# Kernel optimization log

Hardware: AMD Instinct MI355X
Metric: run time of the kernel (lower is better)

The kernel has to match this reference:

```python
import jax, jax.numpy as jnp
import numpy as np

N1 = 50000; N2 = 50000; F = 256; HID = 64; H = 8; DH = HID // H; L = 2; E = 800000


def setup_inputs() -> dict:
    key = jax.random.key(0)
    ks = jax.random.split(key, 20)
    f32 = jnp.float32
    rn = lambda k, shape, s=0.1: jax.random.normal(k, shape, dtype=f32) * s
    inp = {}
    inp['x1'] = jax.random.normal(ks[0], (N1, F), dtype=f32)
    inp['x2'] = jax.random.normal(ks[1], (N2, F), dtype=f32)
    # row 0 = source node ids, row 1 = destination node ids
    inp['edge12'] = jax.random.randint(ks[2], (2, E), 0, N2)  # n1 -> n2
    inp['edge21'] = jax.random.randint(ks[3], (2, E), 0, N1)  # n2 -> n1
    inp['w_in'] = rn(ks[4], (2, HID, F))
    inp['b_in'] = rn(ks[5], (2, HID))
    inp['kw'] = rn(ks[6], (L, 2, HID, HID)); inp['kb'] = rn(ks[7], (L, 2, HID))
    inp['qw'] = rn(ks[8], (L, 2, HID, HID)); inp['qb'] = rn(ks[9], (L, 2, HID))
    inp['vw'] = rn(ks[10], (L, 2, HID, HID)); inp['vb'] = rn(ks[11], (L, 2, HID))
    inp['aw'] = rn(ks[12], (L, 2, HID, HID)); inp['ab'] = rn(ks[13], (L, 2, HID))
    inp['skip'] = jax.random.normal(ks[14], (L, 2), dtype=f32)
    inp['a_rel'] = rn(ks[15], (L, 2, H, DH, DH), 0.3)
    inp['m_rel'] = rn(ks[16], (L, 2, H, DH, DH), 0.3)
    inp['p_rel'] = jnp.ones((L, 2, H), dtype=f32)
    return inp


def _segment_softmax(logits, seg, n):
    # logits: [E, H], seg: [E] destination ids
    m = jax.ops.segment_max(logits, seg, num_segments=n)
    e = jnp.exp(logits - m[seg])
    s = jax.ops.segment_sum(e, seg, num_segments=n)
    return e / s[seg]


def reference(x1, x2, edge12, edge21, w_in, b_in, kw, kb, qw, qb, vw, vb, aw, ab,
              skip, a_rel, m_rel, p_rel):
    scale = jnp.asarray(1.0 / np.sqrt(DH), x1.dtype)

    def kqv(h, l, t):
        k = (h @ kw[l, t].T + kb[l, t]).reshape(-1, H, DH)
        q = (h @ qw[l, t].T + qb[l, t]).reshape(-1, H, DH)
        v = (h @ vw[l, t].T + vb[l, t]).reshape(-1, H, DH)
        return k, q, v

    def message(k_src, v_src, q_dst, edge, ar, mr, pr, n_dst):
        kr = jnp.einsum('nhd,hde->nhe', k_src, ar)   # per-node relation projection
        vr = jnp.einsum('nhd,hde->nhe', v_src, mr)
        s, d = edge[0], edge[1]
        logit = jnp.einsum('ehd,ehd->eh', q_dst[d], kr[s]) * pr[None, :] * scale
        alpha = _segment_softmax(logit, d, n_dst)     # [E, H]
        out = jax.ops.segment_sum(alpha[:, :, None] * vr[s], d, num_segments=n_dst)
        return out.reshape(n_dst, HID)

    def update(o, h, l, t):
        o = jax.nn.gelu(o, approximate=False) @ aw[l, t].T + ab[l, t]
        beta = jax.nn.sigmoid(skip[l, t])
        return beta * o + (1.0 - beta) * h

    # per-node-type input Linear + ReLU stem
    h1 = jax.nn.relu(x1 @ w_in[0].T + b_in[0])
    h2 = jax.nn.relu(x2 @ w_in[1].T + b_in[1])

    outs1, outs2 = [], []
    for l in range(L):
        k1, q1, v1 = kqv(h1, l, 0)
        k2, q2, v2 = kqv(h2, l, 1)
        o2 = message(k1, v1, q2, edge12, a_rel[l, 0], m_rel[l, 0], p_rel[l, 0], h2.shape[0])
        o1 = message(k2, v2, q1, edge21, a_rel[l, 1], m_rel[l, 1], p_rel[l, 1], h1.shape[0])
        h1 = update(o1, h1, l, 0)
        h2 = update(o2, h2, l, 1)
        outs1.append(h1)
        outs2.append(h2)

    Em = jnp.concatenate(outs1, axis=1)  # [N1, HID*L]
    Ed = jnp.concatenate(outs2, axis=1)  # [N2, HID*L]
    return Em, Ed
```

## Files before the change

### kernel.cpp

```cpp
#include <hip/hip_runtime.h>
#include <hip/hip_bf16.h>
#include <hip/hip_fp8.h>
#include <math.h>

typedef __attribute__((ext_vector_type(8))) short bf16x8;
typedef __attribute__((ext_vector_type(4))) float f32x4;
typedef __attribute__((ext_vector_type(2))) float f32x2;
typedef __attribute__((ext_vector_type(4))) unsigned int u32x4;
typedef __attribute__((ext_vector_type(4))) int i32x4;
typedef unsigned short ushort_t;
typedef unsigned char uchar_t;

#define BUCKET_SHIFT 6
#define BUCKET_CAP   64

__device__ inline short f2b(float f) {
    __hip_bfloat16 h = __float2bfloat16(f);
    return __builtin_bit_cast(short, h);
}
__device__ inline float b2f(unsigned short u) {
    return __builtin_bit_cast(float, (unsigned int)u << 16);
}
__device__ inline float blo(unsigned int w) {
    return __builtin_bit_cast(float, w << 16);
}
__device__ inline float bhi(unsigned int w) {
    return __builtin_bit_cast(float, w & 0xffff0000u);
}
__device__ inline uchar_t f2f8(float f) {
    __hip_fp8_e4m3 h(f);
    return (uchar_t)h.__x;
}
__device__ inline float gelu1(float o) {
    return 0.5f * o * (1.f + erff(o * 0.70710678118654752f));
}

__global__ __launch_bounds__(256) void prep_kernel(
    const float* __restrict__ w_in,
    const float* __restrict__ kw, const float* __restrict__ kb,
    const float* __restrict__ qw, const float* __restrict__ qb,
    const float* __restrict__ vw, const float* __restrict__ vb,
    const float* __restrict__ aw,
    const float* __restrict__ a_rel, const float* __restrict__ m_rel,
    const float* __restrict__ p_rel,
    short* __restrict__ wstem, short* __restrict__ Wcat,
    float* __restrict__ Bcat, short* __restrict__ Awb)
{
    int bid = blockIdx.x, tid = threadIdx.x;
    if (bid >= 4) {
        int t = bid - 4;
        for (int i = tid; i < 16384; i += 256)
            wstem[t * 16384 + i] = f2b(w_in[t * 16384 + i]);
        return;
    }
    int base = bid;
    const float* KW = kw + base * 4096;
    const float* QW = qw + base * 4096;
    const float* VW = vw + base * 4096;
    const float* AR = a_rel + base * 512;
    const float* MR = m_rel + base * 512;
    const float* PR = p_rel + base * 8;
    short* WC = Wcat + base * 12288;
    float* BC = Bcat + base * 192;

    for (int i = tid; i < 4096; i += 256) WC[i] = f2b(QW[i]);
    for (int i = tid; i < 4096; i += 256) {
        int out = i >> 6, in = i & 63;
        int h = out >> 3, e = out & 7;
        float s = PR[h] * 0.35355339059327373f;
        float acc = 0.f;
        #pragma unroll
        for (int d = 0; d < 8; ++d) acc += KW[(h * 8 + d) * 64 + in] * AR[h * 64 + d * 8 + e];
        WC[4096 + i] = f2b(acc * s);
    }
    for (int i = tid; i < 4096; i += 256) {
        int out = i >> 6, in = i & 63;
        int h = out >> 3, e = out & 7;
        float acc = 0.f;
        #pragma unroll
        for (int d = 0; d < 8; ++d) acc += VW[(h * 8 + d) * 64 + in] * MR[h * 64 + d * 8 + e];
        WC[8192 + i] = f2b(acc);
    }
    if (tid < 64) {
        BC[tid] = qb[base * 64 + tid];
    } else if (tid < 128) {
        int out = tid - 64;
        int h = out >> 3, e = out & 7;
        float s = PR[h] * 0.35355339059327373f;
        float acc = 0.f;
        #pragma unroll
        for (int d = 0; d < 8; ++d) acc += kb[base * 64 + h * 8 + d] * AR[h * 64 + d * 8 + e];
        BC[64 + out] = acc * s;
    } else if (tid < 192) {
        int out = tid - 128;
        int h = out >> 3, e = out & 7;
        float acc = 0.f;
        #pragma unroll
        for (int d = 0; d < 8; ++d) acc += vb[base * 64 + h * 8 + d] * MR[h * 64 + d * 8 + e];
        BC[128 + out] = acc;
    }
    for (int i = tid; i < 4096; i += 256) Awb[base * 4096 + i] = f2b(aw[base * 4096 + i]);
}

__global__ __launch_bounds__(256) void stem2_mfma(
    const float* __restrict__ X1, const float* __restrict__ X2,
    const short* __restrict__ Wb, const float* __restrict__ B1, const float* __restrict__ B2,
    short* __restrict__ H1, short* __restrict__ H2, int N1, int N2, int nt1)
{
    const float* X; const short* Wsrc; const float* B; short* Hb; int N; int tb;
    if (blockIdx.x < nt1) { X = X1; Wsrc = Wb;         B = B1; Hb = H1; N = N1; tb = blockIdx.x; }
    else                  { X = X2; Wsrc = Wb + 16384; B = B2; Hb = H2; N = N2; tb = blockIdx.x - nt1; }
    __shared__ short Ws[64 * 256];
    int tid = threadIdx.x;
    #pragma unroll
    for (int k = 0; k < 8; ++k) {
        int u = tid + k * 256;
        int row = u >> 5, c = u & 31;
        u32x4 v = *reinterpret_cast<const u32x4*>(Wsrc + row * 256 + c * 8);
        *reinterpret_cast<u32x4*>(&Ws[row * 256 + ((c ^ (row & 7)) << 3)]) = v;
    }
    __syncthreads();
    int w = tid >> 6, l = tid & 63;
    int g = l >> 4, q = l & 15;
    int row = tb * 64 + w * 16 + q;
    bool rok = row < N;
    f32x4 acc[4] = {};
    const float* xr = X + (size_t)row * 256 + g * 8;
    #pragma unroll
    for (int s = 0; s < 8; ++s) {
        bf16x8 a = {};
        if (rok) {
            float4 x0 = *reinterpret_cast<const float4*>(xr + s * 32);
            float4 x1 = *reinterpret_cast<const float4*>(xr + s * 32 + 4);
            a[0] = f2b(x0.x); a[1] = f2b(x0.y); a[2] = f2b(x0.z); a[3] = f2b(x0.w);
            a[4] = f2b(x1.x); a[5] = f2b(x1.y); a[6] = f2b(x1.z); a[7] = f2b(x1.w);
        }
        #pragma unroll
        for (int n = 0; n < 4; ++n) {
            int br = n * 16 + q;
            int c = s * 4 + g;
            bf16x8 b = *reinterpret_cast<bf16x8*>(&Ws[br * 256 + ((c ^ (br & 7)) << 3)]);
            acc[n] = __builtin_amdgcn_mfma_f32_16x16x32_bf16(a, b, acc[n], 0, 0, 0);
        }
    }
    int orow0 = tb * 64 + w * 16 + g * 4;
    #pragma unroll
    for (int n = 0; n < 4; ++n) {
        int col = n * 16 + q;
        float bias = B[col];
        #pragma unroll
        for (int r = 0; r < 4; ++r) {
            int orow = orow0 + r;
            if (orow < N)
                Hb[(size_t)orow * 64 + col] = f2b(fmaxf(acc[n][r] + bias, 0.f));
        }
    }
}

__global__ __launch_bounds__(256) void kqv2_mfma(
    const short* __restrict__ H1, const short* __restrict__ Wc1, const float* __restrict__ Bc1,
    short* __restrict__ Q1, uchar_t* __restrict__ KV1, int N1,
    const short* __restrict__ H2, const short* __restrict__ Wc2, const float* __restrict__ Bc2,
    short* __restrict__ Q2, uchar_t* __restrict__ KV2, int N2, int nt1)
{
    const short* Hb; const short* Wcat; const float* Bcat; short* Qb; uchar_t* KV; int N; int tb;
    if (blockIdx.x < nt1) { Hb = H1; Wcat = Wc1; Bcat = Bc1; Qb = Q1; KV = KV1; N = N1; tb = blockIdx.x; }
    else                  { Hb = H2; Wcat = Wc2; Bcat = Bc2; Qb = Q2; KV = KV2; N = N2; tb = blockIdx.x - nt1; }
    __shared__ short Ws[192 * 64];
    int tid = threadIdx.x;
    #pragma unroll
    for (int k = 0; k < 6; ++k) {
        int u = tid + k * 256;
        int row = u >> 3, c = u & 7;
        u32x4 v = *reinterpret_cast<const u32x4*>(Wcat + row * 64 + c * 8);
        *reinterpret_cast<u32x4*>(&Ws[row * 64 + ((c ^ (row & 7)) << 3)]) = v;
    }
    __syncthreads();
    int w = tid >> 6, l = tid & 63;
    int g = l >> 4, q = l & 15;
    int arow = tb * 64 + w * 16 + q;
    bool rok = arow < N;
    bf16x8 a0 = {}, a1 = {};
    if (rok) {
        a0 = *reinterpret_cast<const bf16x8*>(Hb + (size_t)arow * 64 + g * 8);
        a1 = *reinterpret_cast<const bf16x8*>(Hb + (size_t)arow * 64 + 32 + g * 8);
    }
    f32x4 acc[12] = {};
    #pragma unroll
    for (int n = 0; n < 12; ++n) {
        int br = n * 16 + q;
        bf16x8 b0 = *reinterpret_cast<bf16x8*>(&Ws[br * 64 + ((0 * 4 + g) ^ (br & 7)) * 8]);
        acc[n] = __builtin_amdgcn_mfma_f32_16x16x32_bf16(a0, b0, acc[n], 0, 0, 0);
        bf16x8 b1 = *reinterpret_cast<bf16x8*>(&Ws[br * 64 + ((1 * 4 + g) ^ (br & 7)) * 8]);
        acc[n] = __builtin_amdgcn_mfma_f32_16x16x32_bf16(a1, b1, acc[n], 0, 0, 0);
    }
    int orow0 = tb * 64 + w * 16 + g * 4;
    #pragma unroll
    for (int n = 0; n < 12; ++n) {
        int col = n * 16 + q;
        float bias = Bcat[col];
        #pragma unroll
        for (int r = 0; r < 4; ++r) {
            int orow = orow0 + r;
            if (orow < N) {
                float v = acc[n][r] + bias;
                if (n < 4)      Qb[(size_t)orow * 64 + col]              = f2b(v);
                else if (n < 8) KV[(size_t)orow * 128 + 2 * (col - 64)]  = f2f8(v);
                else            KV[(size_t)orow * 128 + 2 * (col - 128) + 1] = f2f8(v);
            }
        }
    }
}

__global__ __launch_bounds__(256) void bucket8d_kernel(
    const int* __restrict__ e12, const int* __restrict__ e21,
    int* __restrict__ cnt12, int* __restrict__ cnt21,
    ushort_t* __restrict__ cs12, ushort_t* __restrict__ cs21,
    int E, int N1, int N2, int G)
{
    int grp = blockIdx.x & 7;
    int blk = blockIdx.x >> 3;
    bool dirA = grp < 4;
    const int* srcp = dirA ? e12 : e21;
    const int* dstp = dirA ? (e12 + E) : (e21 + E);
    int* cnt = dirA ? cnt12 : cnt21;
    ushort_t* cs = dirA ? cs12 : cs21;
    int Nn = dirA ? N2 : N1;
    int qr = grp & 3;
    int range = (Nn + 3) >> 2;
    int lo = qr * range, hi = lo + range;
    int E4 = E >> 2;
    int stride = G * 256;
    for (int v = blk * 256 + threadIdx.x; v < E4; v += stride) {
        i32x4 d4 = __builtin_nontemporal_load(reinterpret_cast<const i32x4*>(dstp) + v);
        int base = v * 4;
        if (d4.x >= lo && d4.x < hi) { int p = atomicAdd(&cnt[d4.x], 1); if (p < BUCKET_CAP) cs[((size_t)d4.x << BUCKET_SHIFT) + p] = (ushort_t)srcp[base]; }
        if (d4.y >= lo && d4.y < hi) { int p = atomicAdd(&cnt[d4.y], 1); if (p < BUCKET_CAP) cs[((size_t)d4.y << BUCKET_SHIFT) + p] = (ushort_t)srcp[base + 1]; }
        if (d4.z >= lo && d4.z < hi) { int p = atomicAdd(&cnt[d4.z], 1); if (p < BUCKET_CAP) cs[((size_t)d4.z << BUCKET_SHIFT) + p] = (ushort_t)srcp[base + 2]; }
        if (d4.w >= lo && d4.w < hi) { int p = atomicAdd(&cnt[d4.w], 1); if (p < BUCKET_CAP) cs[((size_t)d4.w << BUCKET_SHIFT) + p] = (ushort_t)srcp[base + 3]; }
    }
    int tail = E & 3;
    if (blk == 0 && threadIdx.x < tail) {
        int i = E - tail + threadIdx.x;
        int d = dstp[i];
        if (d >= lo && d < hi) { int p = atomicAdd(&cnt[d], 1); if (p < BUCKET_CAP) cs[((size_t)d << BUCKET_SHIFT) + p] = (ushort_t)srcp[i]; }
    }
}

__global__ __launch_bounds__(256) void gather64_kernel(
    const int* __restrict__ cntA, const ushort_t* __restrict__ csA,
    const short* __restrict__ QA, const uchar_t* __restrict__ KVA, short* __restrict__ GA, int NA,
    const int* __restrict__ cntB, const ushort_t* __restrict__ csB,
    const short* __restrict__ QB, const uchar_t* __restrict__ KVB, short* __restrict__ GB, int NB)
{
    int grp = blockIdx.x & 7;
    int localBlock = (blockIdx.x >> 3) * 4 + (grp & 3);
    const int* cnt; const ushort_t* cs; const short* Qb; const uchar_t* KV; short* G; int N;
    if (grp < 4) { cnt = cntA; cs = csA; Qb = QA; KV = KVA; G = GA; N = NA; }
    else         { cnt = cntB; cs = csB; Qb = QB; KV = KVB; G = GB; N = NB; }
    int d = localBlock * 4 + (threadIdx.x >> 6);
    if (d >= N) return;
    int lane = threadIdx.x & 63;
    int j = lane & 7;
    int sub = lane >> 3;
    int deg = min(cnt[d], BUCKET_CAP);
    u32x4 qw = *reinterpret_cast<const u32x4*>(Qb + (size_t)d * 64 + 8 * j);
    float q0 = blo(qw.x), q1 = bhi(qw.x), q2 = blo(qw.y), q3 = bhi(qw.y);
    float q4 = blo(qw.z), q5 = bhi(qw.z), q6 = blo(qw.w), q7 = bhi(qw.w);
    float a0 = 0.f, a1 = 0.f, a2 = 0.f, a3 = 0.f;
    float a4 = 0.f, a5 = 0.f, a6 = 0.f, a7 = 0.f, den = 0.f;
    int idv = (lane < deg) ? (int)cs[((size_t)d << BUCKET_SHIFT) + lane] : 0;
    for (int i = 0; i < deg; i += 8) {
        int idx = i + sub;
        bool valid = idx < deg;
        int s = __shfl(idv, valid ? idx : 0);
        u32x4 wv = *reinterpret_cast<const u32x4*>(KV + (size_t)s * 128 + 16 * j);
        f32x2 p0 = __builtin_amdgcn_cvt_pk_f32_fp8((int)wv.x, false);
        f32x2 p1 = __builtin_amdgcn_cvt_pk_f32_fp8((int)wv.x, true);
        f32x2 p2 = __builtin_amdgcn_cvt_pk_f32_fp8((int)wv.y, false);
        f32x2 p3 = __builtin_amdgcn_cvt_pk_f32_fp8((int)wv.y, true);
        f32x2 p4 = __builtin_amdgcn_cvt_pk_f32_fp8((int)wv.z, false);
        f32x2 p5 = __builtin_amdgcn_cvt_pk_f32_fp8((int)wv.z, true);
        f32x2 p6 = __builtin_amdgcn_cvt_pk_f32_fp8((int)wv.w, false);
        f32x2 p7 = __builtin_amdgcn_cvt_pk_f32_fp8((int)wv.w, true);
        float t = q0 * p0[0];
        t = fmaf(q1, p1[0], t);
        t = fmaf(q2, p2[0], t);
        t = fmaf(q3, p3[0], t);
        t = fmaf(q4, p4[0], t);
        t = fmaf(q5, p5[0], t);
        t = fmaf(q6, p6[0], t);
        t = fmaf(q7, p7[0], t);
        float e = valid ? __expf(t) : 0.f;
        den += e;
        a0 = fmaf(e, p0[1], a0);
        a1 = fmaf(e, p1[1], a1);
        a2 = fmaf(e, p2[1], a2);
        a3 = fmaf(e, p3[1], a3);
        a4 = fmaf(e, p4[1], a4);
        a5 = fmaf(e, p5[1], a5);
        a6 = fmaf(e, p6[1], a6);
        a7 = fmaf(e, p7[1], a7);
    }
    #pragma unroll
    for (int m = 8; m <= 32; m <<= 1) {
        a0 += __shfl_xor(a0, m); a1 += __shfl_xor(a1, m);
        a2 += __shfl_xor(a2, m); a3 += __shfl_xor(a3, m);
        a4 += __shfl_xor(a4, m); a5 += __shfl_xor(a5, m);
        a6 += __shfl_xor(a6, m); a7 += __shfl_xor(a7, m);
        den += __shfl_xor(den, m);
    }
    if (lane < 8) {
        float r = (den > 0.f) ? 1.f / den : 0.f;
        float g0 = gelu1(a0 * r), g1 = gelu1(a1 * r), g2 = gelu1(a2 * r), g3 = gelu1(a3 * r);
        float g4 = gelu1(a4 * r), g5 = gelu1(a5 * r), g6 = gelu1(a6 * r), g7 = gelu1(a7 * r);
        u32x4 pw;
        pw.x = ((unsigned int)(unsigned short)f2b(g0)) | (((unsigned int)(unsigned short)f2b(g1)) << 16);
        pw.y = ((unsigned int)(unsigned short)f2b(g2)) | (((unsigned int)(unsigned short)f2b(g3)) << 16);
        pw.z = ((unsigned int)(unsigned short)f2b(g4)) | (((unsigned int)(unsigned short)f2b(g5)) << 16);
        pw.w = ((unsigned int)(unsigned short)f2b(g6)) | (((unsigned int)(unsigned short)f2b(g7)) << 16);
        *reinterpret_cast<u32x4*>(G + (size_t)d * 64 + 8 * j) = pw;
    }
}

__global__ __launch_bounds__(256) void updkqv_mfma(
    const short* __restrict__ G1, const short* __restrict__ Aw1, const float* __restrict__ Ab1,
    const float* __restrict__ sk1, short* __restrict__ H1, float* __restrict__ Out1, int N1,
    const short* __restrict__ G2, const short* __restrict__ Aw2, const float* __restrict__ Ab2,
    const float* __restrict__ sk2, short* __restrict__ H2, float* __restrict__ Out2, int N2,
    const short* __restrict__ Wc1n, const float* __restrict__ Bc1n,
    short* __restrict__ Q1, uchar_t* __restrict__ KV1,
    const short* __restrict__ Wc2n, const float* __restrict__ Bc2n,
    short* __restrict__ Q2, uchar_t* __restrict__ KV2,
    int nt1, int outColOff)
{
    const short* G; const short* Awb; const float* Ab; const float* skipp;
    short* Hb; float* Out; int N; int tb;
    const short* Wcat; const float* Bcat; short* Qb; uchar_t* KV;
    if (blockIdx.x < nt1) {
        G = G1; Awb = Aw1; Ab = Ab1; skipp = sk1; Hb = H1; Out = Out1; N = N1; tb = blockIdx.x;
        Wcat = Wc1n; Bcat = Bc1n; Qb = Q1; KV = KV1;
    } else {
        G = G2; Awb = Aw2; Ab = Ab2; skipp = sk2; Hb = H2; Out = Out2; N = N2; tb = blockIdx.x - nt1;
        Wcat = Wc2n; Bcat = Bc2n; Qb = Q2; KV = KV2;
    }
    __shared__ short Ws[192 * 64];
    __shared__ short hs[64][64];
    int tid = threadIdx.x;
    #pragma unroll
    for (int k = 0; k < 6; ++k) {
        int u = tid + k * 256;
        int row = u >> 3, c = u & 7;
        u32x4 v = *reinterpret_cast<const u32x4*>(Wcat + row * 64 + c * 8);
        *reinterpret_cast<u32x4*>(&Ws[row * 64 + ((c ^ (row & 7)) << 3)]) = v;
    }
    int w = tid >> 6, l = tid & 63;
    int g = l >> 4, q = l & 15;
    bf16x8 bfw[4][2];
    #pragma unroll
    for (int n = 0; n < 4; ++n)
        #pragma unroll
        for (int s = 0; s < 2; ++s)
            bfw[n][s] = *reinterpret_cast<const bf16x8*>(Awb + (n * 16 + q) * 64 + s * 32 + g * 8);
    float beta = 1.f / (1.f + __expf(-skipp[0]));
    int arow = tb * 64 + w * 16 + q;
    bool rok = arow < N;
    bf16x8 ua0 = {}, ua1 = {};
    if (rok) {
        ua0 = *reinterpret_cast<const bf16x8*>(G + (size_t)arow * 64 + g * 8);
        ua1 = *reinterpret_cast<const bf16x8*>(G + (size_t)arow * 64 + 32 + g * 8);
    }
    f32x4 uacc[4] = {};
    #pragma unroll
    for (int n = 0; n < 4; ++n) {
        uacc[n] = __builtin_amdgcn_mfma_f32_16x16x32_bf16(ua0, bfw[n][0], uacc[n], 0, 0, 0);
        uacc[n] = __builtin_amdgcn_mfma_f32_16x16x32_bf16(ua1, bfw[n][1], uacc[n], 0, 0, 0);
    }
    int orow0 = tb * 64 + w * 16 + g * 4;
    int lrow0 = w * 16 + g * 4;
    #pragma unroll
    for (int n = 0; n < 4; ++n) {
        int col = n * 16 + q;
        float bias = Ab[col];
        #pragma unroll
        for (int r = 0; r < 4; ++r) {
            int orow = orow0 + r;
            if (orow < N) {
                float hold = b2f(((const unsigned short*)Hb)[(size_t)orow * 64 + col]);
                float hnew = beta * (uacc[n][r] + bias) + (1.f - beta) * hold;
                short hb16 = f2b(hnew);
                Out[(size_t)orow * 128 + outColOff + col] = hnew;
                Hb[(size_t)orow * 64 + col] = hb16;
                hs[lrow0 + r][col] = hb16;
            } else {
                hs[lrow0 + r][col] = 0;
            }
        }
    }
    __syncthreads();
    bf16x8 a0 = *reinterpret_cast<const bf16x8*>(&hs[w * 16 + q][g * 8]);
    bf16x8 a1 = *reinterpret_cast<const bf16x8*>(&hs[w * 16 + q][32 + g * 8]);
    f32x4 acc[12] = {};
    #pragma unroll
    for (int n = 0; n < 12; ++n) {
        int br = n * 16 + q;
        bf16x8 b0 = *reinterpret_cast<bf16x8*>(&Ws[br * 64 + ((0 * 4 + g) ^ (br & 7)) * 8]);
        acc[n] = __builtin_amdgcn_mfma_f32_16x16x32_bf16(a0, b0, acc[n], 0, 0, 0);
        bf16x8 b1 = *reinterpret_cast<bf16x8*>(&Ws[br * 64 + ((1 * 4 + g) ^ (br & 7)) * 8]);
        acc[n] = __builtin_amdgcn_mfma_f32_16x16x32_bf16(a1, b1, acc[n], 0, 0, 0);
    }
    #pragma unroll
    for (int n = 0; n < 12; ++n) {
        int col = n * 16 + q;
        float bias = Bcat[col];
        #pragma unroll
        for (int r = 0; r < 4; ++r) {
            int orow = orow0 + r;
            if (orow < N) {
                float v = acc[n][r] + bias;
                if (n < 4)      Qb[(size_t)orow * 64 + col]              = f2b(v);
                else if (n < 8) KV[(size_t)orow * 128 + 2 * (col - 64)]  = f2f8(v);
                else            KV[(size_t)orow * 128 + 2 * (col - 128) + 1] = f2f8(v);
            }
        }
    }
}

__global__ __launch_bounds__(256) void update2_mfma(
    const short* __restrict__ G1, const short* __restrict__ Aw1, const float* __restrict__ Ab1,
    const float* __restrict__ sk1, short* __restrict__ H1, float* __restrict__ Out1, int N1,
    const short* __restrict__ G2, const short* __restrict__ Aw2, const float* __restrict__ Ab2,
    const float* __restrict__ sk2, short* __restrict__ H2, float* __restrict__ Out2, int N2,
    int nt1, int outColOff)
{
    const short* G; const short* Awb; const float* Ab; const float* skipp;
    short* Hb; float* Out; int N; int tb;
    if (blockIdx.x < nt1) { G = G1; Awb = Aw1; Ab = Ab1; skipp = sk1; Hb = H1; Out = Out1; N = N1; tb = blockIdx.x; }
    else                  { G = G2; Awb = Aw2; Ab = Ab2; skipp = sk2; Hb = H2; Out = Out2; N = N2; tb = blockIdx.x - nt1; }
    int tid = threadIdx.x;
    int w = tid >> 6, l = tid & 63;
    int g = l >> 4, q = l & 15;
    bf16x8 bf[4][2];
    #pragma unroll
    for (int n = 0; n < 4; ++n)
        #pragma unroll
        for (int s = 0; s < 2; ++s)
            bf[n][s] = *reinterpret_cast<const bf16x8*>(Awb + (n * 16 + q) * 64 + s * 32 + g * 8);
    float beta = 1.f / (1.f + __expf(-skipp[0]));
    int arow = tb * 64 + w * 16 + q;
    bool rok = arow < N;
    bf16x8 a0 = {}, a1 = {};
    if (rok) {
        a0 = *reinterpret_cast<const bf16x8*>(G + (size_t)arow * 64 + g * 8);
        a1 = *reinterpret_cast<const bf16x8*>(G + (size_t)arow * 64 + 32 + g * 8);
    }
    f32x4 acc[4] = {};
    #pragma unroll
    for (int n = 0; n < 4; ++n) {
        acc[n] = __builtin_amdgcn_mfma_f32_16x16x32_bf16(a0, bf[n][0], acc[n], 0, 0, 0);
        acc[n] = __builtin_amdgcn_mfma_f32_16x16x32_bf16(a1, bf[n][1], acc[n], 0, 0, 0);
    }
    int orow0 = tb * 64 + w * 16 + g * 4;
    #pragma unroll
    for (int n = 0; n < 4; ++n) {
        int col = n * 16 + q;
        float bias = Ab[col];
        #pragma unroll
        for (int r = 0; r < 4; ++r) {
            int orow = orow0 + r;
            if (orow < N) {
                float hold = b2f(((const unsigned short*)Hb)[(size_t)orow * 64 + col]);
                float hnew = beta * (acc[n][r] + bias) + (1.f - beta) * hold;
                Out[(size_t)orow * 128 + outColOff + col] = hnew;
                Hb[(size_t)orow * 64 + col] = f2b(hnew);
            }
        }
    }
}

extern "C" void kernel_launch(void* const* d_in, const int* in_sizes, int n_in,
                              void* d_out, int out_size, void* d_ws, size_t ws_size,
                              hipStream_t stream) {
    const float* x1    = (const float*)d_in[0];
    const float* x2    = (const float*)d_in[1];
    const int*   e12   = (const int*)d_in[2];
    const int*   e21   = (const int*)d_in[3];
    const float* w_in  = (const float*)d_in[4];
    const float* b_in  = (const float*)d_in[5];
    const float* kw    = (const float*)d_in[6];
    const float* kb    = (const float*)d_in[7];
    const float* qw    = (const float*)d_in[8];
    const float* qb    = (const float*)d_in[9];
    const float* vw    = (const float*)d_in[10];
    const float* vb    = (const float*)d_in[11];
    const float* aw    = (const float*)d_in[12];
    const float* ab    = (const float*)d_in[13];
    const float* skip  = (const float*)d_in[14];
    const float* a_rel = (const float*)d_in[15];
    const float* m_rel = (const float*)d_in[16];
    const float* p_rel = (const float*)d_in[17];

    int N1 = in_sizes[0] / 256;
    int N2 = in_sizes[1] / 256;
    int E  = in_sizes[2] / 2;

    float* out = (float*)d_out;

    char* wsp = (char*)d_ws;
    auto alloc = [&](size_t bytes) { void* p = wsp; wsp += (bytes + 255) & ~(size_t)255; return p; };
    short* hb1   = (short*)alloc((size_t)N1 * 64 * 2);
    short* hb2   = (short*)alloc((size_t)N2 * 64 * 2);
    short* qb1   = (short*)alloc((size_t)N1 * 64 * 2);
    short* qb2   = (short*)alloc((size_t)N2 * 64 * 2);
    uchar_t* kv1 = (uchar_t*)alloc((size_t)N1 * 128);
    uchar_t* kv2 = (uchar_t*)alloc((size_t)N2 * 128);
    short* g1    = (short*)alloc((size_t)N1 * 64 * 2);
    short* g2    = (short*)alloc((size_t)N2 * 64 * 2);
    short* wstem = (short*)alloc(2 * 16384 * 2);
    short* WcatB = (short*)alloc(4 * 12288 * 2);
    float* BcatB = (float*)alloc(4 * 192 * 4);
    short* AwbB  = (short*)alloc(4 * 4096 * 2);
    int* cnts    = (int*)alloc((size_t)(N1 + N2) * 4);
    int* cnt12   = cnts;
    int* cnt21   = cnts + N2;
    ushort_t* csr12 = (ushort_t*)alloc(((size_t)N2 << BUCKET_SHIFT) * 2);
    ushort_t* csr21 = (ushort_t*)alloc(((size_t)N1 << BUCKET_SHIFT) * 2);

    const int BLK = 256;
    int nt1 = (N1 + 63) / 64;
    int nt2 = (N2 + 63) / 64;
    const int G8 = 512;

    prep_kernel<<<6, BLK, 0, stream>>>(w_in, kw, kb, qw, qb, vw, vb, aw,
                                       a_rel, m_rel, p_rel, wstem, WcatB, BcatB, AwbB);

    hipMemsetAsync(cnts, 0, (size_t)(N1 + N2) * 4, stream);
    bucket8d_kernel<<<8 * G8, BLK, 0, stream>>>(e12, e21, cnt12, cnt21,
                                                csr12, csr21, E, N1, N2, G8);

    stem2_mfma<<<nt1 + nt2, BLK, 0, stream>>>(x1, x2, wstem, b_in, b_in + 64,
                                              hb1, hb2, N1, N2, nt1);

    int bA = (N2 + 3) / 4;
    int bB = (N1 + 3) / 4;
    int bmax = bA > bB ? bA : bB;
    int nlb = (bmax + 3) / 4;
    int gblocks = 8 * nlb;

    kqv2_mfma<<<nt1 + nt2, BLK, 0, stream>>>(
        hb1, WcatB + (size_t)0 * 12288, BcatB + (size_t)0 * 192, qb1, kv1, N1,
        hb2, WcatB + (size_t)1 * 12288, BcatB + (size_t)1 * 192, qb2, kv2, N2, nt1);

    gather64_kernel<<<gblocks, BLK, 0, stream>>>(
        cnt12, csr12, qb2, kv1, g2, N2,
        cnt21, csr21, qb1, kv2, g1, N1);

    updkqv_mfma<<<nt1 + nt2, BLK, 0, stream>>>(
        g1, AwbB + (size_t)0 * 4096, ab + (size_t)0 * 64, skip + 0, hb1, out, N1,
        g2, AwbB + (size_t)1 * 4096, ab + (size_t)1 * 64, skip + 1, hb2,
        out + (size_t)N1 * 128, N2,
        WcatB + (size_t)2 * 12288, BcatB + (size_t)2 * 192, qb1, kv1,
        WcatB + (size_t)3 * 12288, BcatB + (size_t)3 * 192, qb2, kv2,
        nt1, 0);

    gather64_kernel<<<gblocks, BLK, 0, stream>>>(
        cnt12, csr12, qb2, kv1, g2, N2,
        cnt21, csr21, qb1, kv2, g1, N1);

    update2_mfma<<<nt1 + nt2, BLK, 0, stream>>>(
        g1, AwbB + (size_t)2 * 4096, ab + (size_t)2 * 64, skip + 2, hb1, out, N1,
        g2, AwbB + (size_t)3 * 4096, ab + (size_t)3 * 64, skip + 3, hb2,
        out + (size_t)N1 * 128, N2, nt1, 64);
}
```

Baseline: 296.3 us.

## Replace atomic bucket scatter with two-pass LDS radix partition of edges

Swaps the single-pass bucketing kernel, which used global atomics per edge and scattered 2-byte writes, for a two-pass partition. Pass A reads edge chunks, builds a block-local histogram over 256-node destination buckets, and writes packed payloads contiguously into per-bucket global regions. Pass B loads each bucket's payload, builds the 64-slot per-node lists in LDS with shared atomics, and writes them out with coalesced vector stores. The goal is to cut scattered global atomic and store traffic. The cost is an extra kernel launch, a payload round trip through memory, and a fixed per-bucket capacity (RCAP) that silently drops edges if a bucket overflows.

```diff
diff --git a/kernel.cpp b/kernel.cpp
--- a/kernel.cpp
+++ b/kernel.cpp
@@ -13,6 +13,8 @@
 
 #define BUCKET_SHIFT 6
 #define BUCKET_CAP   64
+#define CHUNK        4096
+#define RCAP         4608
 
 __device__ inline short f2b(float f) {
     __hip_bfloat16 h = __float2bfloat16(f);
@@ -212,39 +214,111 @@
     }
 }
 
-__global__ __launch_bounds__(256) void bucket8d_kernel(
+__global__ __launch_bounds__(256) void partA_kernel(
     const int* __restrict__ e12, const int* __restrict__ e21,
-    int* __restrict__ cnt12, int* __restrict__ cnt21,
-    ushort_t* __restrict__ cs12, ushort_t* __restrict__ cs21,
-    int E, int N1, int N2, int G)
-{
-    int grp = blockIdx.x & 7;
-    int blk = blockIdx.x >> 3;
-    bool dirA = grp < 4;
-    const int* srcp = dirA ? e12 : e21;
-    const int* dstp = dirA ? (e12 + E) : (e21 + E);
-    int* cnt = dirA ? cnt12 : cnt21;
-    ushort_t* cs = dirA ? cs12 : cs21;
-    int Nn = dirA ? N2 : N1;
-    int qr = grp & 3;
-    int range = (Nn + 3) >> 2;
-    int lo = qr * range, hi = lo + range;
-    int E4 = E >> 2;
-    int stride = G * 256;
-    for (int v = blk * 256 + threadIdx.x; v < E4; v += stride) {
-        i32x4 d4 = __builtin_nontemporal_load(reinterpret_cast<const i32x4*>(dstp) + v);
-        int base = v * 4;
-        if (d4.x >= lo && d4.x < hi) { int p = atomicAdd(&cnt[d4.x], 1); if (p < BUCKET_CAP) cs[((size_t)d4.x << BUCKET_SHIFT) + p] = (ushort_t)srcp[base]; }
-        if (d4.y >= lo && d4.y < hi) { int p = atomicAdd(&cnt[d4.y], 1); if (p < BUCKET_CAP) cs[((size_t)d4.y << BUCKET_SHIFT) + p] = (ushort_t)srcp[base + 1]; }
-        if (d4.z >= lo && d4.z < hi) { int p = atomicAdd(&cnt[d4.z], 1); if (p < BUCKET_CAP) cs[((size_t)d4.z << BUCKET_SHIFT) + p] = (ushort_t)srcp[base + 2]; }
-        if (d4.w >= lo && d4.w < hi) { int p = atomicAdd(&cnt[d4.w], 1); if (p < BUCKET_CAP) cs[((size_t)d4.w << BUCKET_SHIFT) + p] = (ushort_t)srcp[base + 3]; }
-    }
-    int tail = E & 3;
-    if (blk == 0 && threadIdx.x < tail) {
-        int i = E - tail + threadIdx.x;
-        int d = dstp[i];
-        if (d >= lo && d < hi) { int p = atomicAdd(&cnt[d], 1); if (p < BUCKET_CAP) cs[((size_t)d << BUCKET_SHIFT) + p] = (ushort_t)srcp[i]; }
-    }
+    unsigned int* __restrict__ gpay, int* __restrict__ gcur,
+    int E, int nbA, int nbB, int NA)
+{
+    bool dirB = blockIdx.x >= NA;
+    int cb = dirB ? blockIdx.x - NA : blockIdx.x;
+    const int* srcp = dirB ? e21 : e12;
+    const int* dstp = srcp + E;
+    int nb = dirB ? nbB : nbA;
+    int goff = dirB ? nbA : 0;
+    __shared__ int hist[256];
+    __shared__ int lstart[256];
+    __shared__ int gbase[256];
+    __shared__ int scanb[256];
+    __shared__ unsigned int pay[CHUNK];
+    int tid = threadIdx.x;
+    hist[tid] = 0;
+    __syncthreads();
+    int base = cb * CHUNK;
+    int dstv[16], srcv[16];
+    #pragma unroll
+    for (int k = 0; k < 16; ++k) {
+        int i = base + tid + k * 256;
+        if (i < E) {
+            dstv[k] = dstp[i];
+            srcv[k] = srcp[i];
+            atomicAdd(&hist[dstv[k] >> 8], 1);
+        } else {
+            dstv[k] = -1;
+            srcv[k] = 0;
+        }
+    }
+    __syncthreads();
+    int v = hist[tid];
+    scanb[tid] = v;
+    __syncthreads();
+    for (int off = 1; off < 256; off <<= 1) {
+        int t2 = (tid >= off) ? scanb[tid - off] : 0;
+        __syncthreads();
+        scanb[tid] += t2;
+        __syncthreads();
+    }
+    lstart[tid] = scanb[tid] - v;
+    __syncthreads();
+    hist[tid] = lstart[tid];
+    __syncthreads();
+    #pragma unroll
+    for (int k = 0; k < 16; ++k) {
+        if (dstv[k] >= 0) {
+            int bk = dstv[k] >> 8;
+            int pos = atomicAdd(&hist[bk], 1);
+            pay[pos] = ((unsigned int)bk << 24) | ((unsigned int)(dstv[k] & 255) << 16)
+                     | (unsigned int)srcv[k];
+        }
+    }
+    __syncthreads();
+    int mycnt = hist[tid] - lstart[tid];
+    if (tid < nb && mycnt > 0) gbase[tid] = atomicAdd(&gcur[goff + tid], mycnt);
+    else gbase[tid] = 0;
+    __syncthreads();
+    int total = min(CHUNK, E - base);
+    for (int i = tid; i < total; i += 256) {
+        unsigned int e = pay[i];
+        int bk = e >> 24;
+        int idx = i - lstart[bk];
+        int p = gbase[bk] + idx;
+        if (p < RCAP)
+            gpay[(size_t)(goff + bk) * RCAP + p] = e;
+    }
+}
+
+__global__ __launch_bounds__(256) void partB_kernel(
+    const unsigned int* __restrict__ gpay, const int* __restrict__ gcur,
+    ushort_t* __restrict__ cs12, int* __restrict__ cnt12, int N2,
+    ushort_t* __restrict__ cs21, int* __restrict__ cnt21, int N1, int nbA)
+{
+    bool dirB = blockIdx.x >= nbA;
+    int bk = dirB ? blockIdx.x - nbA : blockIdx.x;
+    ushort_t* cs = dirB ? cs21 : cs12;
+    int* cnt = dirB ? cnt21 : cnt12;
+    int Nd = dirB ? N1 : N2;
+    int gi = dirB ? nbA + bk : bk;
+    __shared__ int lcnt[256];
+    __shared__ ushort_t lcs[256 * 64];
+    int tid = threadIdx.x;
+    lcnt[tid] = 0;
+    __syncthreads();
+    int n = min(gcur[gi], RCAP);
+    const unsigned int* pay = gpay + (size_t)gi * RCAP;
+    for (int i = tid; i < n; i += 256) {
+        unsigned int e = pay[i];
+        int dl = (e >> 16) & 255;
+        int pos = atomicAdd(&lcnt[dl], 1);
+        if (pos < BUCKET_CAP) lcs[(dl << 6) + pos] = (ushort_t)(e & 0xffff);
+    }
+    __syncthreads();
+    int d0 = bk << 8;
+    int nrow = min(256, Nd - d0);
+    if (nrow <= 0) return;
+    const u32x4* lsrc = reinterpret_cast<const u32x4*>(lcs);
+    u32x4* gdst = reinterpret_cast<u32x4*>(cs + ((size_t)d0 << 6));
+    int nu = nrow << 3;
+    for (int u = tid; u < nu; u += 256) gdst[u] = lsrc[u];
+    if (tid < nrow) cnt[d0 + tid] = min(lcnt[tid], BUCKET_CAP);
 }
 
 __global__ __launch_bounds__(256) void gather64_kernel(
@@ -520,23 +594,28 @@
     short* WcatB = (short*)alloc(4 * 12288 * 2);
     float* BcatB = (float*)alloc(4 * 192 * 4);
     short* AwbB  = (short*)alloc(4 * 4096 * 2);
-    int* cnts    = (int*)alloc((size_t)(N1 + N2) * 4);
-    int* cnt12   = cnts;
-    int* cnt21   = cnts + N2;
+    int* cnt12   = (int*)alloc((size_t)N2 * 4);
+    int* cnt21   = (int*)alloc((size_t)N1 * 4);
     ushort_t* csr12 = (ushort_t*)alloc(((size_t)N2 << BUCKET_SHIFT) * 2);
     ushort_t* csr21 = (ushort_t*)alloc(((size_t)N1 << BUCKET_SHIFT) * 2);
+
+    int nbA = (N2 + 255) >> 8;
+    int nbB = (N1 + 255) >> 8;
+    int* gcur = (int*)alloc((size_t)(nbA + nbB) * 4);
+    unsigned int* gpay = (unsigned int*)alloc((size_t)(nbA + nbB) * RCAP * 4);
 
     const int BLK = 256;
     int nt1 = (N1 + 63) / 64;
     int nt2 = (N2 + 63) / 64;
-    const int G8 = 512;
+    int NA = (E + CHUNK - 1) / CHUNK;
 
     prep_kernel<<<6, BLK, 0, stream>>>(w_in, kw, kb, qw, qb, vw, vb, aw,
                                        a_rel, m_rel, p_rel, wstem, WcatB, BcatB, AwbB);
 
-    hipMemsetAsync(cnts, 0, (size_t)(N1 + N2) * 4, stream);
-    bucket8d_kernel<<<8 * G8, BLK, 0, stream>>>(e12, e21, cnt12, cnt21,
-                                                csr12, csr21, E, N1, N2, G8);
+    hipMemsetAsync(gcur, 0, (size_t)(nbA + nbB) * 4, stream);
+    partA_kernel<<<2 * NA, BLK, 0, stream>>>(e12, e21, gpay, gcur, E, nbA, nbB, NA);
+    partB_kernel<<<nbA + nbB, BLK, 0, stream>>>(gpay, gcur, csr12, cnt12, N2,
+                                                csr21, cnt21, N1, nbA);
 
     stem2_mfma<<<nt1 + nt2, BLK, 0, stream>>>(x1, x2, wstem, b_in, b_in + 64,
                                               hb1, hb2, N1, N2, nt1);
```

Result: faster. 252.3 us (-14.9%).
